# Kernel tuning notes

Hardware: AMD Instinct MI355X
Metric: run time of the kernel (lower is better)

## Reference

```python
import jax, jax.numpy as jnp
import numpy as np

L, H, NH, NKV, HD, FF, V = 2, 2048, 16, 2, 128, 11008, 32000
B, S, R, LORA_SCALE = 32, 64, 16, 2.0  # lora scaling = alpha/r = 32/16
PH, TD = 1024, 512
ROPE_THETA = 1e6

def _rms(x, w, eps=1e-6):
    return x * jax.lax.rsqrt(jnp.mean(x * x, axis=-1, keepdims=True) + eps) * w

def _rot_half(x):
    h = x.shape[-1] // 2
    return jnp.concatenate([-x[..., h:], x[..., :h]], axis=-1)

def _lora_linear(x, W, A, Bm, b=None):
    y = x @ W.T + LORA_SCALE * ((x @ A.T) @ Bm.T)
    return y + b if b is not None else y

def _forward(input_ids, attention_mask, embed, Wq, bq, Aq, Bq, Wk, bk, Ak, Bk,
             Wv, bv, Av, Bv, Wo, Ao, Bo, ln1, ln2, Wg, Wu, Wd, norm_f,
             W1, b1, W2, b2):
    Bsz, Sl = input_ids.shape
    h = embed[input_ids]                                            # [B,S,H]
    inv_freq = 1.0 / (ROPE_THETA ** (jnp.arange(0, HD, 2, dtype=jnp.float32) / HD))
    ang = jnp.arange(Sl, dtype=jnp.float32)[:, None] * inv_freq      # [S,HD/2]
    cos = jnp.concatenate([jnp.cos(ang)] * 2, -1)[None, :, None, :]  # [1,S,1,HD]
    sin = jnp.concatenate([jnp.sin(ang)] * 2, -1)[None, :, None, :]
    causal = jnp.tril(jnp.ones((Sl, Sl), dtype=bool))
    keep = causal[None, None] & (attention_mask[:, None, None, :] > 0)
    bias = jnp.where(keep, 0.0, -1e9).astype(jnp.float32)            # [B,1,S,S]
    for l in range(L):
        x = _rms(h, ln1[l])
        q = _lora_linear(x, Wq[l], Aq[l], Bq[l], bq[l]).reshape(Bsz, Sl, NH, HD)
        k = _lora_linear(x, Wk[l], Ak[l], Bk[l], bk[l]).reshape(Bsz, Sl, NKV, HD)
        v = _lora_linear(x, Wv[l], Av[l], Bv[l], bv[l]).reshape(Bsz, Sl, NKV, HD)
        q = q * cos + _rot_half(q) * sin
        k = k * cos + _rot_half(k) * sin
        k = jnp.repeat(k, NH // NKV, axis=2)                         # GQA expand
        v = jnp.repeat(v, NH // NKV, axis=2)
        scores = jnp.einsum('bqhd,bkhd->bhqk', q, k) / np.sqrt(HD).astype(np.float32) + bias
        p = jax.nn.softmax(scores, axis=-1)
        attn = jnp.einsum('bhqk,bkhd->bqhd', p, v).reshape(Bsz, Sl, H)
        h = h + _lora_linear(attn, Wo[l], Ao[l], Bo[l])
        x = _rms(h, ln2[l])
        h = h + (jax.nn.silu(x @ Wg[l].T) * (x @ Wu[l].T)) @ Wd[l].T  # SwiGLU MLP
    h = _rms(h, norm_f)                       # final norm -> hidden_states[-1]
    seq_len = jnp.sum(attention_mask, axis=1) - 1
    pooled = h[jnp.arange(Bsz), seq_len]      # last valid token  [B,H]
    z = jax.nn.gelu(pooled @ W1.T + b1, approximate=False)
    return (z @ W2.T + b2).astype(jnp.float32)  # [B,512]

def setup_inputs():
    key = jax.random.key(0)
    ks = jax.random.split(key, 32)
    def n(k, shape, s=0.02):
        return (s * jax.random.normal(k, shape)).astype(jnp.float32)
    lens = jax.random.randint(ks[0], (B,), 1, S + 1)
    return {
        'input_ids': jax.random.randint(ks[1], (B, S), 0, V, dtype=jnp.int32),
        'attention_mask': (jnp.arange(S)[None, :] < lens[:, None]).astype(jnp.int32),
        'embed': n(ks[2], (V, H)),
        'Wq': n(ks[3], (L, H, H)), 'bq': n(ks[4], (L, H)),
        'Aq': n(ks[5], (L, R, H)), 'Bq': n(ks[6], (L, H, R)),
        'Wk': n(ks[7], (L, NKV * HD, H)), 'bk': n(ks[8], (L, NKV * HD)),
        'Ak': n(ks[9], (L, R, H)), 'Bk': n(ks[10], (L, NKV * HD, R)),
        'Wv': n(ks[11], (L, NKV * HD, H)), 'bv': n(ks[12], (L, NKV * HD)),
        'Av': n(ks[13], (L, R, H)), 'Bv': n(ks[14], (L, NKV * HD, R)),
        'Wo': n(ks[15], (L, H, H)),
        'Ao': n(ks[16], (L, R, H)), 'Bo': n(ks[17], (L, H, R)),
        'ln1': jnp.ones((L, H), jnp.float32), 'ln2': jnp.ones((L, H), jnp.float32),
        'Wg': n(ks[18], (L, FF, H)), 'Wu': n(ks[19], (L, FF, H)), 'Wd': n(ks[20], (L, H, FF)),
        'norm_f': jnp.ones((H,), jnp.float32),
        'W1': n(ks[21], (PH, H)), 'b1': jnp.zeros((PH,), jnp.float32),
        'W2': n(ks[22], (TD, PH)), 'b2': jnp.zeros((TD,), jnp.float32),
    }

def reference(input_ids, attention_mask, embed, Wq, bq, Aq, Bq, Wk, bk, Ak, Bk,
              Wv, bv, Av, Bv, Wo, Ao, Bo, ln1, ln2, Wg, Wu, Wd, norm_f,
              W1, b1, W2, b2):
    return _forward(input_ids, attention_mask, embed, Wq, bq, Aq, Bq, Wk, bk, Ak, Bk,
                    Wv, bv, Av, Bv, Wo, Ao, Bo, ln1, ln2, Wg, Wu, Wd, norm_f,
                    W1, b1, W2, b2)
```

## Files before the change

kernel.cpp:

```cpp
#include <hip/hip_runtime.h>
#include <hip/hip_bf16.h>
#include <math.h>

namespace {
constexpr int NL  = 2;
constexpr int H   = 2048;
constexpr int NH  = 16;
constexpr int NKV = 2;
constexpr int HD  = 128;
constexpr int FF  = 11008;
constexpr int BB  = 32;
constexpr int SS  = 64;
constexpr int RR  = 16;
constexpr int TT  = BB * SS;
constexpr int KVD = NKV * HD;
constexpr int QKVD = H + 2 * KVD;
constexpr int PH  = 1024, TDm = 512;
constexpr float LSCALE = 2.0f;
}

typedef __bf16 bf16x8 __attribute__((ext_vector_type(8)));
typedef float  f32x4  __attribute__((ext_vector_type(4)));

__device__ __forceinline__ ushort4 f4_to_bf4(float4 r) {
  __hip_bfloat16 a = __float2bfloat16(r.x), b = __float2bfloat16(r.y),
                 c = __float2bfloat16(r.z), d = __float2bfloat16(r.w);
  return make_ushort4(*(unsigned short*)&a, *(unsigned short*)&b,
                      *(unsigned short*)&c, *(unsigned short*)&d);
}

__global__ __launch_bounds__(256) void k_embed(const int* __restrict__ ids,
                                               const float* __restrict__ emb,
                                               float* __restrict__ h) {
  int t = blockIdx.x;
  long id = ids[t];
  const float4* src = reinterpret_cast<const float4*>(emb + id * (long)H);
  float4* dst = reinterpret_cast<float4*>(h + (long)t * H);
  for (int i = threadIdx.x; i < H / 4; i += 256) dst[i] = src[i];
}

__global__ __launch_bounds__(256) void k_cvt(const float* __restrict__ src,
                                             __hip_bfloat16* __restrict__ dst, long n) {
  long i = ((long)blockIdx.x * 256 + threadIdx.x) * 4;
  if (i >= n) return;
  float4 v = *reinterpret_cast<const float4*>(src + i);
  *reinterpret_cast<ushort4*>(dst + i) = f4_to_bf4(v);
}

__global__ __launch_bounds__(256) void k_rmsnorm(const float* __restrict__ in,
                                                 const float* __restrict__ w,
                                                 float* __restrict__ out,
                                                 __hip_bfloat16* __restrict__ outb) {
  int t = blockIdx.x, tid = threadIdx.x;
  const float4* xr = reinterpret_cast<const float4*>(in + (long)t * H);
  float4 v0 = xr[tid], v1 = xr[tid + 256];
  float ss = v0.x*v0.x + v0.y*v0.y + v0.z*v0.z + v0.w*v0.w
           + v1.x*v1.x + v1.y*v1.y + v1.z*v1.z + v1.w*v1.w;
  #pragma unroll
  for (int off = 32; off; off >>= 1) ss += __shfl_xor(ss, off);
  __shared__ float sred[4];
  if ((tid & 63) == 0) sred[tid >> 6] = ss;
  __syncthreads();
  float scale = rsqrtf((sred[0] + sred[1] + sred[2] + sred[3]) * (1.0f / H) + 1e-6f);
  const float4* wr = reinterpret_cast<const float4*>(w);
  float4 w0 = wr[tid], w1 = wr[tid + 256];
  float4 r0 = make_float4(v0.x*scale*w0.x, v0.y*scale*w0.y, v0.z*scale*w0.z, v0.w*scale*w0.w);
  float4 r1 = make_float4(v1.x*scale*w1.x, v1.y*scale*w1.y, v1.z*scale*w1.z, v1.w*scale*w1.w);
  float4* o = reinterpret_cast<float4*>(out + (long)t * H);
  o[tid] = r0; o[tid + 256] = r1;
  ushort4* ob = reinterpret_cast<ushort4*>(outb + (long)t * H);
  ob[tid] = f4_to_bf4(r0); ob[tid + 256] = f4_to_bf4(r1);
}

enum { ME_BIAS_F32 = 0, ME_ACC_F32 = 1, ME_SILU_BF16 = 2, ME_MUL_BF16 = 3 };

__device__ __forceinline__ int raster_sw(int bid, int nwg) {
  int q8 = nwg >> 3, r8 = nwg & 7;
  int xcd = bid & 7, pos = bid >> 3;
  return (xcd < r8 ? xcd * (q8 + 1) : r8 * (q8 + 1) + (xcd - r8) * q8) + pos;
}

template <int EPI>
__global__ __launch_bounds__(512) void k_mgemm(
    const __hip_bfloat16* __restrict__ Abf,
    const __hip_bfloat16* __restrict__ Wbf,
    const float* __restrict__ bias,
    float* __restrict__ Cf,
    __hip_bfloat16* Cb,
    const __hip_bfloat16* gate,
    int M, int N, int K) {
  constexpr int BM = 128, BN = 128, BK = 32;
  constexpr int FM = 4, FN = 2;
  constexpr int ACH = BM * BK / 8, BCH = BN * BK / 8;
  __shared__ __align__(16) __bf16 As[2][BM * BK];
  __shared__ __align__(16) __bf16 Bs[2][BN * BK];
  const int tid = threadIdx.x;
  const int sw = raster_sw(blockIdx.x, gridDim.x);
  const int ntm = M / BM;
  const int bm = (sw % ntm) * BM, bn = (sw / ntm) * BN;
  const int lane = tid & 63, wv = tid >> 6;
  const int wm = (wv >> 2) * 64, wn = (wv & 3) * 32;
  const int lr15 = lane & 15;
  const int lks = (((lane >> 4) << 3)) ^ ((((lr15 >> 1) & 3)) << 3);
  f32x4 acc[FM][FN] = {};
  const __bf16* Ag = reinterpret_cast<const __bf16*>(Abf) + (long)bm * K;
  const __bf16* Bg = reinterpret_cast<const __bf16*>(Wbf) + (long)bn * K;

  auto stage = [&](int buf, int k0) {
    #pragma unroll
    for (int i = tid; i < ACH; i += 512)
      __builtin_amdgcn_global_load_lds(
          (const __attribute__((address_space(1))) void*)
            (Ag + (long)(i >> 2) * K + k0 + (((i & 3) ^ ((i >> 3) & 3)) << 3)),
          (__attribute__((address_space(3))) void*)(&As[buf][i * 8]), 16, 0, 0);
    #pragma unroll
    for (int i = tid; i < BCH; i += 512)
      __builtin_amdgcn_global_load_lds(
          (const __attribute__((address_space(1))) void*)
            (Bg + (long)(i >> 2) * K + k0 + (((i & 3) ^ ((i >> 3) & 3)) << 3)),
          (__attribute__((address_space(3))) void*)(&Bs[buf][i * 8]), 16, 0, 0);
  };
  auto compute = [&](int buf) {
    bf16x8 af[FM], bfr[FN];
    #pragma unroll
    for (int m = 0; m < FM; ++m)
      af[m] = *reinterpret_cast<const bf16x8*>(&As[buf][(wm + m * 16 + lr15) * BK + lks]);
    #pragma unroll
    for (int n = 0; n < FN; ++n)
      bfr[n] = *reinterpret_cast<const bf16x8*>(&Bs[buf][(wn + n * 16 + lr15) * BK + lks]);
    #pragma unroll
    for (int m = 0; m < FM; ++m)
      #pragma unroll
      for (int n = 0; n < FN; ++n)
        acc[m][n] = __builtin_amdgcn_mfma_f32_16x16x32_bf16(af[m], bfr[n], acc[m][n], 0, 0, 0);
  };

  stage(0, 0);
  asm volatile("s_waitcnt vmcnt(0)" ::: "memory");
  __builtin_amdgcn_s_barrier();
  int cur = 0;
  for (int k0 = BK; k0 < K; k0 += BK) {
    stage(cur ^ 1, k0);
    compute(cur);
    asm volatile("s_waitcnt vmcnt(0)" ::: "memory");
    __builtin_amdgcn_s_barrier();
    cur ^= 1;
  }
  compute(cur);

  const int r0 = (lane >> 4) << 2;
  #pragma unroll
  for (int m = 0; m < FM; ++m)
    #pragma unroll
    for (int n = 0; n < FN; ++n) {
      const int col = bn + wn + n * 16 + lr15;
      const long rowb = bm + wm + m * 16 + r0;
      #pragma unroll
      for (int j = 0; j < 4; ++j) {
        const long off = (rowb + j) * N + col;
        float v = acc[m][n][j];
        if constexpr (EPI == ME_BIAS_F32) {
          Cf[off] = v + bias[col];
        } else if constexpr (EPI == ME_ACC_F32) {
          Cf[off] += v;
        } else if constexpr (EPI == ME_SILU_BF16) {
          Cb[off] = __float2bfloat16(v / (1.0f + expf(-v)));
        } else {
          float g = __bfloat162float(gate[off]);
          Cb[off] = __float2bfloat16(v * g);
        }
      }
    }
}

template <int BM, int BN, int WROWS, int WCOLS>
__global__ __launch_bounds__(256, 2) void k_swiglu(
    const __hip_bfloat16* __restrict__ Abf,
    const __hip_bfloat16* __restrict__ Wgb,
    const __hip_bfloat16* __restrict__ Wub,
    __hip_bfloat16* __restrict__ Cb,
    int M, int N, int K) {
  constexpr int BK = 32;
  constexpr int WTM = BM / WROWS, WTN = BN / WCOLS;
  constexpr int FM = WTM / 16, FN = WTN / 16;
  constexpr int ACH = BM * BK / 8, BCH = BN * BK / 8;
  __shared__ __align__(16) __bf16 As[2][BM * BK];
  __shared__ __align__(16) __bf16 Gs[2][BN * BK];
  __shared__ __align__(16) __bf16 Us[2][BN * BK];
  const int tid = threadIdx.x;
  const int sw = raster_sw(blockIdx.x, gridDim.x);
  const int ntm = M / BM;
  const int bm = (sw % ntm) * BM, bn = (sw / ntm) * BN;
  const int lane = tid & 63, wv = tid >> 6;
  const int wm = (wv / WCOLS) * WTM, wn = (wv % WCOLS) * WTN;
  const int lr15 = lane & 15;
  const int lks = (((lane >> 4) << 3)) ^ ((((lr15 >> 1) & 3)) << 3);
  f32x4 accg[FM][FN] = {}, accu[FM][FN] = {};
  const __bf16* Ag = reinterpret_cast<const __bf16*>(Abf) + (long)bm * K;
  const __bf16* Gg = reinterpret_cast<const __bf16*>(Wgb) + (long)bn * K;
  const __bf16* Ug = reinterpret_cast<const __bf16*>(Wub) + (long)bn * K;

  auto stage = [&](int buf, int k0) {
    #pragma unroll
    for (int i = tid; i < ACH; i += 256)
      __builtin_amdgcn_global_load_lds(
          (const __attribute__((address_space(1))) void*)
            (Ag + (long)(i >> 2) * K + k0 + (((i & 3) ^ ((i >> 3) & 3)) << 3)),
          (__attribute__((address_space(3))) void*)(&As[buf][i * 8]), 16, 0, 0);
    #pragma unroll
    for (int i = tid; i < BCH; i += 256)
      __builtin_amdgcn_global_load_lds(
          (const __attribute__((address_space(1))) void*)
            (Gg + (long)(i >> 2) * K + k0 + (((i & 3) ^ ((i >> 3) & 3)) << 3)),
          (__attribute__((address_space(3))) void*)(&Gs[buf][i * 8]), 16, 0, 0);
    #pragma unroll
    for (int i = tid; i < BCH; i += 256)
      __builtin_amdgcn_global_load_lds(
          (const __attribute__((address_space(1))) void*)
            (Ug + (long)(i >> 2) * K + k0 + (((i & 3) ^ ((i >> 3) & 3)) << 3)),
          (__attribute__((address_space(3))) void*)(&Us[buf][i * 8]), 16, 0, 0);
  };
  auto compute = [&](int buf) {
    bf16x8 af[FM], gf[FN], uf[FN];
    #pragma unroll
    for (int m = 0; m < FM; ++m)
      af[m] = *reinterpret_cast<const bf16x8*>(&As[buf][(wm + m * 16 + lr15) * BK + lks]);
    #pragma unroll
    for (int n = 0; n < FN; ++n) {
      gf[n] = *reinterpret_cast<const bf16x8*>(&Gs[buf][(wn + n * 16 + lr15) * BK + lks]);
      uf[n] = *reinterpret_cast<const bf16x8*>(&Us[buf][(wn + n * 16 + lr15) * BK + lks]);
    }
    #pragma unroll
    for (int m = 0; m < FM; ++m)
      #pragma unroll
      for (int n = 0; n < FN; ++n) {
        accg[m][n] = __builtin_amdgcn_mfma_f32_16x16x32_bf16(af[m], gf[n], accg[m][n], 0, 0, 0);
        accu[m][n] = __builtin_amdgcn_mfma_f32_16x16x32_bf16(af[m], uf[n], accu[m][n], 0, 0, 0);
      }
  };

  stage(0, 0);
  asm volatile("s_waitcnt vmcnt(0)" ::: "memory");
  __builtin_amdgcn_s_barrier();
  int cur = 0;
  for (int k0 = BK; k0 < K; k0 += BK) {
    stage(cur ^ 1, k0);
    compute(cur);
    asm volatile("s_waitcnt vmcnt(0)" ::: "memory");
    __builtin_amdgcn_s_barrier();
    cur ^= 1;
  }
  compute(cur);

  const int r0 = (lane >> 4) << 2;
  #pragma unroll
  for (int m = 0; m < FM; ++m)
    #pragma unroll
    for (int n = 0; n < FN; ++n) {
      const int col = bn + wn + n * 16 + lr15;
      const long rowb = bm + wm + m * 16 + r0;
      #pragma unroll
      for (int j = 0; j < 4; ++j) {
        float g = accg[m][n][j], u = accu[m][n][j];
        Cb[(rowb + j) * N + col] = __float2bfloat16((g / (1.0f + expf(-g))) * u);
      }
    }
}

enum { EPI_STORE = 0, EPI_GELU = 3 };

template <int EPI, bool HAS_BIAS>
__global__ __launch_bounds__(256) void k_gemm(const float* __restrict__ A,
                                              const float* __restrict__ W,
                                              const float* __restrict__ bias,
                                              float* __restrict__ C,
                                              int M, int N, int K) {
  constexpr int BM = 64, BN = 64, BK = 16;
  __shared__ float As[BK][BM + 4];
  __shared__ float Ws[BK][BN + 4];
  const int bm = blockIdx.y * BM, bn = blockIdx.x * BN;
  const int tid = threadIdx.x;
  const int lr = tid >> 2;
  const int lc = (tid & 3) << 2;
  const int ty = tid >> 4, tx = tid & 15;
  float acc[4][4] = {};
  const int arow = bm + lr;
  const bool aok = arow < M;
  const float* Ap = A + (long)arow * K + lc;
  const float* Wp = W + (long)(bn + lr) * K + lc;
  for (int k0 = 0; k0 < K; k0 += BK) {
    float4 av = aok ? *reinterpret_cast<const float4*>(Ap + k0) : make_float4(0.f, 0.f, 0.f, 0.f);
    float4 wv = *reinterpret_cast<const float4*>(Wp + k0);
    As[lc + 0][lr] = av.x; As[lc + 1][lr] = av.y; As[lc + 2][lr] = av.z; As[lc + 3][lr] = av.w;
    Ws[lc + 0][lr] = wv.x; Ws[lc + 1][lr] = wv.y; Ws[lc + 2][lr] = wv.z; Ws[lc + 3][lr] = wv.w;
    __syncthreads();
    #pragma unroll
    for (int k = 0; k < BK; ++k) {
      float4 a4 = *reinterpret_cast<const float4*>(&As[k][ty << 2]);
      float4 b4 = *reinterpret_cast<const float4*>(&Ws[k][tx << 2]);
      float a[4] = {a4.x, a4.y, a4.z, a4.w};
      float b[4] = {b4.x, b4.y, b4.z, b4.w};
      #pragma unroll
      for (int i = 0; i < 4; ++i)
        #pragma unroll
        for (int j = 0; j < 4; ++j) acc[i][j] = fmaf(a[i], b[j], acc[i][j]);
    }
    __syncthreads();
  }
  const int col = bn + (tx << 2);
  #pragma unroll
  for (int i = 0; i < 4; ++i) {
    int row = bm + (ty << 2) + i;
    if (row < M) {
      float4 r = make_float4(acc[i][0], acc[i][1], acc[i][2], acc[i][3]);
      if (HAS_BIAS) {
        float4 bv = *reinterpret_cast<const float4*>(bias + col);
        r.x += bv.x; r.y += bv.y; r.z += bv.z; r.w += bv.w;
      }
      if (EPI == EPI_GELU) {
        r.x = 0.5f * r.x * (1.0f + erff(r.x * 0.70710678118654752f));
        r.y = 0.5f * r.y * (1.0f + erff(r.y * 0.70710678118654752f));
        r.z = 0.5f * r.z * (1.0f + erff(r.z * 0.70710678118654752f));
        r.w = 0.5f * r.w * (1.0f + erff(r.w * 0.70710678118654752f));
      }
      *reinterpret_cast<float4*>(C + (long)row * N + col) = r;
    }
  }
}

__global__ __launch_bounds__(256) void k_lora_down(const float* __restrict__ x,
                                                   const float* __restrict__ A,
                                                   float* __restrict__ tmp) {
  int t = blockIdx.x, tid = threadIdx.x;
  int r = tid & 15, sl = tid >> 4;
  const float* xr = x + (long)t * H + sl * 128;
  const float* Ar = A + (long)r * H + sl * 128;
  float p = 0.f;
  #pragma unroll 8
  for (int kk = 0; kk < 128; kk += 4) {
    float4 xv = *reinterpret_cast<const float4*>(xr + kk);
    float4 av = *reinterpret_cast<const float4*>(Ar + kk);
    p = fmaf(xv.x, av.x, p); p = fmaf(xv.y, av.y, p);
    p = fmaf(xv.z, av.z, p); p = fmaf(xv.w, av.w, p);
  }
  __shared__ float red[16][17];
  red[sl][r] = p;
  __syncthreads();
  if (tid < 16) {
    float s = 0.f;
    #pragma unroll
    for (int i = 0; i < 16; ++i) s += red[i][tid];
    tmp[t * RR + tid] = s;
  }
}

__global__ __launch_bounds__(256) void k_lora_add(const float* __restrict__ tmp,
                                                  const float* __restrict__ Bm,
                                                  float* __restrict__ C, int ldC, int N) {
  long idx = (long)blockIdx.x * 256 + threadIdx.x;
  if (idx >= (long)TT * N) return;
  int t = (int)(idx / N), n = (int)(idx % N);
  const float* tr = tmp + (long)t * RR;
  const float* br = Bm + (long)n * RR;
  float s = 0.f;
  #pragma unroll
  for (int r = 0; r < RR; ++r) s = fmaf(tr[r], br[r], s);
  C[(long)t * ldC + n] += LSCALE * s;
}

__global__ __launch_bounds__(256) void k_rope_tab(float2* __restrict__ tab) {
  int idx = blockIdx.x * 256 + threadIdx.x;
  if (idx >= SS * 64) return;
  int pos = idx >> 6, j = idx & 63;
  float inv = 1.0f / powf(1.0e6f, (float)(2 * j) * (1.0f / HD));
  float ang = (float)pos * inv;
  tab[idx] = make_float2(cosf(ang), sinf(ang));
}

__global__ __launch_bounds__(256) void k_rope(float* __restrict__ qkv,
                                              const float2* __restrict__ tab) {
  int t = blockIdx.x;
  const float2* trow = tab + (t & (SS - 1)) * 64;
  float* row = qkv + (long)t * QKVD;
  for (int idx = threadIdx.x; idx < NH * 64 + NKV * 64; idx += 256) {
    float* base;
    int j;
    if (idx < NH * 64) {
      int head = idx >> 6; j = idx & 63;
      base = row + head * HD;
    } else {
      int i2 = idx - NH * 64;
      int head = i2 >> 6; j = i2 & 63;
      base = row + H + head * HD;
    }
    float2 cs2 = trow[j];
    float lo = base[j], hi = base[j + 64];
    base[j]      = lo * cs2.x - hi * cs2.y;
    base[j + 64] = hi * cs2.x + lo * cs2.y;
  }
}

__global__ __launch_bounds__(64) void k_attn(const float* __restrict__ qkv,
                                             const int* __restrict__ mask,
                                             float* __restrict__ o,
                                             __hip_bfloat16* __restrict__ obf) {
  int flat = blockIdx.x;
  int qi = flat & (SS - 1);
  int hh = (flat >> 6) & (NH - 1);
  int b  = flat >> 10;
  int lane = threadIdx.x;
  int kv = hh >> 3;
  long t = (long)b * SS + qi;
  const float* qr = qkv + t * QKVD + hh * HD;
  const float* kr = qkv + ((long)b * SS + lane) * QKVD + H + kv * HD;
  float dot = 0.f;
  #pragma unroll 8
  for (int d = 0; d < HD; d += 4) {
    float4 qv = *reinterpret_cast<const float4*>(qr + d);
    float4 kvv = *reinterpret_cast<const float4*>(kr + d);
    dot = fmaf(qv.x, kvv.x, dot); dot = fmaf(qv.y, kvv.y, dot);
    dot = fmaf(qv.z, kvv.z, dot); dot = fmaf(qv.w, kvv.w, dot);
  }
  bool keep = (lane <= qi) && (mask[b * SS + lane] > 0);
  float sc = dot * 0.08838834764831845f + (keep ? 0.f : -1e9f);
  float m = sc;
  #pragma unroll
  for (int off = 32; off; off >>= 1) m = fmaxf(m, __shfl_xor(m, off));
  float e = expf(sc - m);
  float s = e;
  #pragma unroll
  for (int off = 32; off; off >>= 1) s += __shfl_xor(s, off);
  float p = e / s;
  __shared__ float pl[64];
  pl[lane] = p;
  __syncthreads();
  float o0 = 0.f, o1 = 0.f;
  const float* vb = qkv + (long)b * SS * QKVD + H + KVD + kv * HD;
  for (int ki = 0; ki < SS; ++ki) {
    float pp = pl[ki];
    o0 = fmaf(pp, vb[(long)ki * QKVD + lane], o0);
    o1 = fmaf(pp, vb[(long)ki * QKVD + lane + 64], o1);
  }
  long oidx = t * H + hh * HD + lane;
  o[oidx] = o0;
  o[oidx + 64] = o1;
  __hip_bfloat16 b0 = __float2bfloat16(o0), b1 = __float2bfloat16(o1);
  obf[oidx] = b0;
  obf[oidx + 64] = b1;
}

__global__ __launch_bounds__(256) void k_pool(const float* __restrict__ x,
                                              const int* __restrict__ mask,
                                              float* __restrict__ pooled) {
  int b = blockIdx.x;
  __shared__ int len;
  if (threadIdx.x == 0) {
    int L2 = 0;
    for (int i = 0; i < SS; ++i) L2 += (mask[b * SS + i] > 0);
    len = L2;
  }
  __syncthreads();
  const float4* sp = reinterpret_cast<const float4*>(x + ((long)b * SS + len - 1) * H);
  float4* dp = reinterpret_cast<float4*>(pooled + (long)b * H);
  for (int i = threadIdx.x; i < H / 4; i += 256) dp[i] = sp[i];
}

static inline int cvt_grid(long n) { return (int)((n / 4 + 255) / 256); }

extern "C" void kernel_launch(void* const* d_in, const int* in_sizes, int n_in,
                              void* d_out, int out_size, void* d_ws, size_t ws_size,
                              hipStream_t stream) {
  const int*   ids    = (const int*)d_in[0];
  const int*   mask   = (const int*)d_in[1];
  const float* embed  = (const float*)d_in[2];
  const float* Wq     = (const float*)d_in[3];
  const float* bq     = (const float*)d_in[4];
  const float* Aq     = (const float*)d_in[5];
  const float* Bq     = (const float*)d_in[6];
  const float* Wk     = (const float*)d_in[7];
  const float* bk     = (const float*)d_in[8];
  const float* Ak     = (const float*)d_in[9];
  const float* Bk     = (const float*)d_in[10];
  const float* Wv     = (const float*)d_in[11];
  const float* bv     = (const float*)d_in[12];
  const float* Av     = (const float*)d_in[13];
  const float* Bv     = (const float*)d_in[14];
  const float* Wo     = (const float*)d_in[15];
  const float* Ao     = (const float*)d_in[16];
  const float* Bo     = (const float*)d_in[17];
  const float* ln1    = (const float*)d_in[18];
  const float* ln2    = (const float*)d_in[19];
  const float* Wg     = (const float*)d_in[20];
  const float* Wu     = (const float*)d_in[21];
  const float* Wd     = (const float*)d_in[22];
  const float* norm_f = (const float*)d_in[23];
  const float* W1     = (const float*)d_in[24];
  const float* b1     = (const float*)d_in[25];
  const float* W2     = (const float*)d_in[26];
  const float* b2     = (const float*)d_in[27];

  float* ws = (float*)d_ws;
  float* h       = ws;
  float* x       = h    + (long)TT * H;
  float* qkv     = x    + (long)TT * H;
  float* tmpR    = qkv  + (long)TT * QKVD;
  float* pooled  = tmpR + (long)TT * RR;
  float* zz      = pooled + (long)BB * H;
  float* biascat = zz   + (long)BB * PH;
  float2* ropetab = (float2*)(biascat + QKVD);
  float* endf32  = (float*)(ropetab + SS * 64);
  __hip_bfloat16* x_bf = (__hip_bfloat16*)endf32;
  __hip_bfloat16* ffbf = x_bf + (long)TT * H;
  __hip_bfloat16* wbf  = ffbf + (long)TT * FF;
  __hip_bfloat16* wbf2 = wbf  + (long)FF * H;
  size_t need_fused = (size_t)((char*)(wbf2 + (long)FF * H) - (char*)d_ws);
  bool fused_ok = ws_size >= need_fused;

  k_embed<<<TT, 256, 0, stream>>>(ids, embed, h);
  k_rope_tab<<<(SS * 64 + 255) / 256, 256, 0, stream>>>(ropetab);

  for (int l = 0; l < NL; ++l) {
    const long lHH = (long)l * H * H;
    const long lKH = (long)l * KVD * H;
    const long lRH = (long)l * RR * H;
    k_rmsnorm<<<TT, 256, 0, stream>>>(h, ln1 + l * H, x, x_bf);
    k_cvt<<<cvt_grid((long)H * H), 256, 0, stream>>>(Wq + lHH, wbf, (long)H * H);
    k_cvt<<<cvt_grid((long)KVD * H), 256, 0, stream>>>(Wk + lKH, wbf + (long)H * H, (long)KVD * H);
    k_cvt<<<cvt_grid((long)KVD * H), 256, 0, stream>>>(Wv + lKH, wbf + (long)(H + KVD) * H, (long)KVD * H);
    hipMemcpyAsync(biascat,           bq + (long)l * H,   H * sizeof(float),   hipMemcpyDeviceToDevice, stream);
    hipMemcpyAsync(biascat + H,       bk + (long)l * KVD, KVD * sizeof(float), hipMemcpyDeviceToDevice, stream);
    hipMemcpyAsync(biascat + H + KVD, bv + (long)l * KVD, KVD * sizeof(float), hipMemcpyDeviceToDevice, stream);
    k_mgemm<ME_BIAS_F32><<<(TT / 128) * (QKVD / 128), 512, 0, stream>>>(
        x_bf, wbf, biascat, qkv, nullptr, nullptr, TT, QKVD, H);
    k_lora_down<<<TT, 256, 0, stream>>>(x, Aq + lRH, tmpR);
    k_lora_add<<<((long)TT * H + 255) / 256, 256, 0, stream>>>(tmpR, Bq + (long)l * H * RR, qkv, QKVD, H);
    k_lora_down<<<TT, 256, 0, stream>>>(x, Ak + lRH, tmpR);
    k_lora_add<<<((long)TT * KVD + 255) / 256, 256, 0, stream>>>(tmpR, Bk + (long)l * KVD * RR, qkv + H, QKVD, KVD);
    k_lora_down<<<TT, 256, 0, stream>>>(x, Av + lRH, tmpR);
    k_lora_add<<<((long)TT * KVD + 255) / 256, 256, 0, stream>>>(tmpR, Bv + (long)l * KVD * RR, qkv + H + KVD, QKVD, KVD);
    k_rope<<<TT, 256, 0, stream>>>(qkv, ropetab);
    k_attn<<<BB * NH * SS, 64, 0, stream>>>(qkv, mask, x, x_bf);
    k_lora_down<<<TT, 256, 0, stream>>>(x, Ao + lRH, tmpR);
    k_cvt<<<cvt_grid((long)H * H), 256, 0, stream>>>(Wo + lHH, wbf, (long)H * H);
    k_mgemm<ME_ACC_F32><<<(TT / 128) * (H / 128), 512, 0, stream>>>(
        x_bf, wbf, nullptr, h, nullptr, nullptr, TT, H, H);
    k_lora_add<<<((long)TT * H + 255) / 256, 256, 0, stream>>>(tmpR, Bo + (long)l * H * RR, h, H, H);
    k_rmsnorm<<<TT, 256, 0, stream>>>(h, ln2 + l * H, x, x_bf);
    if (fused_ok) {
      k_cvt<<<cvt_grid((long)FF * H), 256, 0, stream>>>(Wg + (long)l * FF * H, wbf, (long)FF * H);
      k_cvt<<<cvt_grid((long)FF * H), 256, 0, stream>>>(Wu + (long)l * FF * H, wbf2, (long)FF * H);
      k_swiglu<128, 128, 2, 2><<<(TT / 128) * (FF / 128), 256, 0, stream>>>(
          x_bf, wbf, wbf2, ffbf, TT, FF, H);
    } else {
      k_cvt<<<cvt_grid((long)FF * H), 256, 0, stream>>>(Wg + (long)l * FF * H, wbf, (long)FF * H);
      k_mgemm<ME_SILU_BF16><<<(TT / 128) * (FF / 128), 512, 0, stream>>>(
          x_bf, wbf, nullptr, nullptr, ffbf, nullptr, TT, FF, H);
      k_cvt<<<cvt_grid((long)FF * H), 256, 0, stream>>>(Wu + (long)l * FF * H, wbf, (long)FF * H);
      k_mgemm<ME_MUL_BF16><<<(TT / 128) * (FF / 128), 512, 0, stream>>>(
          x_bf, wbf, nullptr, nullptr, ffbf, ffbf, TT, FF, H);
    }
    k_cvt<<<cvt_grid((long)H * FF), 256, 0, stream>>>(Wd + (long)l * H * FF, wbf, (long)H * FF);
    k_mgemm<ME_ACC_F32><<<(TT / 128) * (H / 128), 512, 0, stream>>>(
        ffbf, wbf, nullptr, h, nullptr, nullptr, TT, H, FF);
  }

  k_rmsnorm<<<TT, 256, 0, stream>>>(h, norm_f, x, x_bf);
  k_pool<<<BB, 256, 0, stream>>>(x, mask, pooled);
  k_gemm<EPI_GELU, true><<<dim3(PH / 64, 1), 256, 0, stream>>>(pooled, W1, b1, zz, BB, PH, H);
  k_gemm<EPI_STORE, true><<<dim3(TDm / 64, 1), 256, 0, stream>>>(zz, W2, b2, (float*)d_out, BB, TDm, PH);
}
```

Baseline: 2.117 ms.

## Convert fp32 weights to bf16 inside GEMM staging and fuse LoRA up-projection into epilogue

```diff
diff --git a/kernel.cpp b/kernel.cpp
--- a/kernel.cpp
+++ b/kernel.cpp
@@ -29,6 +29,17 @@
                       *(unsigned short*)&c, *(unsigned short*)&d);
 }
 
+__device__ __forceinline__ bf16x8 f8cvt(float4 a, float4 b) {
+  bf16x8 r;
+  r[0] = (__bf16)a.x; r[1] = (__bf16)a.y; r[2] = (__bf16)a.z; r[3] = (__bf16)a.w;
+  r[4] = (__bf16)b.x; r[5] = (__bf16)b.y; r[6] = (__bf16)b.z; r[7] = (__bf16)b.w;
+  return r;
+}
+
+__device__ __forceinline__ float dot4(float4 a, float4 b) {
+  return a.x * b.x + a.y * b.y + a.z * b.z + a.w * b.w;
+}
+
 __global__ __launch_bounds__(256) void k_embed(const int* __restrict__ ids,
                                                const float* __restrict__ emb,
                                                float* __restrict__ h) {
@@ -39,12 +50,20 @@
   for (int i = threadIdx.x; i < H / 4; i += 256) dst[i] = src[i];
 }
 
-__global__ __launch_bounds__(256) void k_cvt(const float* __restrict__ src,
-                                             __hip_bfloat16* __restrict__ dst, long n) {
-  long i = ((long)blockIdx.x * 256 + threadIdx.x) * 4;
-  if (i >= n) return;
-  float4 v = *reinterpret_cast<const float4*>(src + i);
-  *reinterpret_cast<ushort4*>(dst + i) = f4_to_bf4(v);
+__global__ __launch_bounds__(256) void k_prep(
+    const float* __restrict__ bq, const float* __restrict__ bk, const float* __restrict__ bv,
+    const float* __restrict__ Bq, const float* __restrict__ Bk, const float* __restrict__ Bv,
+    float* __restrict__ biascat, float* __restrict__ bcat) {
+  int idx = blockIdx.x * 256 + threadIdx.x;
+  if (idx >= NL * QKVD) return;
+  int l = idx / QKVD, col = idx % QKVD;
+  const float* bsrc; const float* Bsrc;
+  if (col < H)            { bsrc = bq + (long)l * H + col;            Bsrc = Bq + ((long)l * H + col) * RR; }
+  else if (col < H + KVD) { bsrc = bk + (long)l * KVD + (col - H);    Bsrc = Bk + ((long)l * KVD + col - H) * RR; }
+  else                    { bsrc = bv + (long)l * KVD + (col - H - KVD); Bsrc = Bv + ((long)l * KVD + col - H - KVD) * RR; }
+  biascat[idx] = *bsrc;
+  #pragma unroll
+  for (int r = 0; r < RR; ++r) bcat[(long)idx * RR + r] = Bsrc[r];
 }
 
 __global__ __launch_bounds__(256) void k_rmsnorm(const float* __restrict__ in,
@@ -72,7 +91,7 @@
   ob[tid] = f4_to_bf4(r0); ob[tid + 256] = f4_to_bf4(r1);
 }
 
-enum { ME_BIAS_F32 = 0, ME_ACC_F32 = 1, ME_SILU_BF16 = 2, ME_MUL_BF16 = 3 };
+enum { ME_BIAS_F32 = 0, ME_ACC_F32 = 1 };
 
 __device__ __forceinline__ int raster_sw(int bid, int nwg) {
   int q8 = nwg >> 3, r8 = nwg & 7;
@@ -80,18 +99,16 @@
   return (xcd < r8 ? xcd * (q8 + 1) : r8 * (q8 + 1) + (xcd - r8) * q8) + pos;
 }
 
-template <int EPI>
+template <int EPI, bool LORA>
 __global__ __launch_bounds__(512) void k_mgemm(
     const __hip_bfloat16* __restrict__ Abf,
-    const __hip_bfloat16* __restrict__ Wbf,
+    const float* __restrict__ W0, const float* __restrict__ W1, const float* __restrict__ W2,
     const float* __restrict__ bias,
     float* __restrict__ Cf,
-    __hip_bfloat16* Cb,
-    const __hip_bfloat16* gate,
-    int M, int N, int K) {
+    const float* __restrict__ lt, const float* __restrict__ lB, int ltStride,
+    int qkvMode, int M, int N, int K) {
   constexpr int BM = 128, BN = 128, BK = 32;
   constexpr int FM = 4, FN = 2;
-  constexpr int ACH = BM * BK / 8, BCH = BN * BK / 8;
   __shared__ __align__(16) __bf16 As[2][BM * BK];
   __shared__ __align__(16) __bf16 Bs[2][BN * BK];
   const int tid = threadIdx.x;
@@ -104,21 +121,29 @@
   const int lks = (((lane >> 4) << 3)) ^ ((((lr15 >> 1) & 3)) << 3);
   f32x4 acc[FM][FN] = {};
   const __bf16* Ag = reinterpret_cast<const __bf16*>(Abf) + (long)bm * K;
-  const __bf16* Bg = reinterpret_cast<const __bf16*>(Wbf) + (long)bn * K;
-
-  auto stage = [&](int buf, int k0) {
-    #pragma unroll
-    for (int i = tid; i < ACH; i += 512)
-      __builtin_amdgcn_global_load_lds(
-          (const __attribute__((address_space(1))) void*)
-            (Ag + (long)(i >> 2) * K + k0 + (((i & 3) ^ ((i >> 3) & 3)) << 3)),
-          (__attribute__((address_space(3))) void*)(&As[buf][i * 8]), 16, 0, 0);
-    #pragma unroll
-    for (int i = tid; i < BCH; i += 512)
-      __builtin_amdgcn_global_load_lds(
-          (const __attribute__((address_space(1))) void*)
-            (Bg + (long)(i >> 2) * K + k0 + (((i & 3) ^ ((i >> 3) & 3)) << 3)),
-          (__attribute__((address_space(3))) void*)(&Bs[buf][i * 8]), 16, 0, 0);
+
+  const float* Wsrc = W0; int wrow0 = bn;
+  if (qkvMode) {
+    if (bn >= H + KVD)      { Wsrc = W2; wrow0 = bn - (H + KVD); }
+    else if (bn >= H)       { Wsrc = W1; wrow0 = bn - H; }
+  }
+  const int brow = tid >> 2, bc = tid & 3;
+  const float* wp = Wsrc + (long)(wrow0 + brow) * K + bc * 8;
+  const int bdst = brow * BK + ((bc ^ ((brow >> 1) & 3)) << 3);
+
+  float4 b0, b1;
+  auto loadB = [&](int k0) {
+    b0 = *reinterpret_cast<const float4*>(wp + k0);
+    b1 = *reinterpret_cast<const float4*>(wp + k0 + 4);
+  };
+  auto writeB = [&](int buf) {
+    *reinterpret_cast<bf16x8*>(&Bs[buf][bdst]) = f8cvt(b0, b1);
+  };
+  auto stageA = [&](int buf, int k0) {
+    __builtin_amdgcn_global_load_lds(
+        (const __attribute__((address_space(1))) void*)
+          (Ag + (long)(tid >> 2) * K + k0 + (((tid & 3) ^ ((tid >> 3) & 3)) << 3)),
+        (__attribute__((address_space(3))) void*)(&As[buf][tid * 8]), 16, 0, 0);
   };
   auto compute = [&](int buf) {
     bf16x8 af[FM], bfr[FN];
@@ -135,55 +160,71 @@
         acc[m][n] = __builtin_amdgcn_mfma_f32_16x16x32_bf16(af[m], bfr[n], acc[m][n], 0, 0, 0);
   };
 
-  stage(0, 0);
-  asm volatile("s_waitcnt vmcnt(0)" ::: "memory");
-  __builtin_amdgcn_s_barrier();
+  const int NS = K / BK;
+  loadB(0);
+  stageA(0, 0);
+  writeB(0);
+  __syncthreads();
   int cur = 0;
-  for (int k0 = BK; k0 < K; k0 += BK) {
-    stage(cur ^ 1, k0);
+  for (int t = 0; t < NS; ++t) {
+    if (t + 1 < NS) { loadB((t + 1) * BK); stageA(cur ^ 1, (t + 1) * BK); }
     compute(cur);
-    asm volatile("s_waitcnt vmcnt(0)" ::: "memory");
-    __builtin_amdgcn_s_barrier();
-    cur ^= 1;
-  }
-  compute(cur);
+    if (t + 1 < NS) {
+      writeB(cur ^ 1);
+      __syncthreads();
+      cur ^= 1;
+    }
+  }
 
   const int r0 = (lane >> 4) << 2;
+  float4 lb[FN][4];
+  int goff = 0;
+  if constexpr (LORA) {
+    if (qkvMode) goff = (bn >= H + KVD) ? 32 : (bn >= H ? 16 : 0);
+    #pragma unroll
+    for (int n = 0; n < FN; ++n) {
+      const float4* p = reinterpret_cast<const float4*>(lB + (long)(bn + wn + n * 16 + lr15) * RR);
+      lb[n][0] = p[0]; lb[n][1] = p[1]; lb[n][2] = p[2]; lb[n][3] = p[3];
+    }
+  }
+  float bcol[FN];
+  if constexpr (EPI == ME_BIAS_F32) {
+    #pragma unroll
+    for (int n = 0; n < FN; ++n) bcol[n] = bias[bn + wn + n * 16 + lr15];
+  }
   #pragma unroll
   for (int m = 0; m < FM; ++m)
     #pragma unroll
-    for (int n = 0; n < FN; ++n) {
-      const int col = bn + wn + n * 16 + lr15;
-      const long rowb = bm + wm + m * 16 + r0;
+    for (int j = 0; j < 4; ++j) {
+      const long row = bm + wm + m * 16 + r0 + j;
+      float lv[FN];
+      if constexpr (LORA) {
+        const float4* tp = reinterpret_cast<const float4*>(lt + row * ltStride + goff);
+        float4 t0 = tp[0], t1 = tp[1], t2 = tp[2], t3 = tp[3];
+        #pragma unroll
+        for (int n = 0; n < FN; ++n)
+          lv[n] = LSCALE * (dot4(t0, lb[n][0]) + dot4(t1, lb[n][1]) +
+                            dot4(t2, lb[n][2]) + dot4(t3, lb[n][3]));
+      }
       #pragma unroll
-      for (int j = 0; j < 4; ++j) {
-        const long off = (rowb + j) * N + col;
+      for (int n = 0; n < FN; ++n) {
+        const int col = bn + wn + n * 16 + lr15;
         float v = acc[m][n][j];
-        if constexpr (EPI == ME_BIAS_F32) {
-          Cf[off] = v + bias[col];
-        } else if constexpr (EPI == ME_ACC_F32) {
-          Cf[off] += v;
-        } else if constexpr (EPI == ME_SILU_BF16) {
-          Cb[off] = __float2bfloat16(v / (1.0f + expf(-v)));
-        } else {
-          float g = __bfloat162float(gate[off]);
-          Cb[off] = __float2bfloat16(v * g);
-        }
+        if constexpr (LORA) v += lv[n];
+        if constexpr (EPI == ME_BIAS_F32) Cf[row * N + col] = v + bcol[n];
+        else                              Cf[row * N + col] += v;
       }
     }
 }
 
-template <int BM, int BN, int WROWS, int WCOLS>
 __global__ __launch_bounds__(256, 2) void k_swiglu(
     const __hip_bfloat16* __restrict__ Abf,
-    const __hip_bfloat16* __restrict__ Wgb,
-    const __hip_bfloat16* __restrict__ Wub,
+    const float* __restrict__ Wg,
+    const float* __restrict__ Wu,
     __hip_bfloat16* __restrict__ Cb,
     int M, int N, int K) {
-  constexpr int BK = 32;
-  constexpr int WTM = BM / WROWS, WTN = BN / WCOLS;
-  constexpr int FM = WTM / 16, FN = WTN / 16;
-  constexpr int ACH = BM * BK / 8, BCH = BN * BK / 8;
+  constexpr int BM = 128, BN = 128, BK = 32;
+  constexpr int FM = 4, FN = 4;
   __shared__ __align__(16) __bf16 As[2][BM * BK];
   __shared__ __align__(16) __bf16 Gs[2][BN * BK];
   __shared__ __align__(16) __bf16 Us[2][BN * BK];
@@ -192,33 +233,45 @@
   const int ntm = M / BM;
   const int bm = (sw % ntm) * BM, bn = (sw / ntm) * BN;
   const int lane = tid & 63, wv = tid >> 6;
-  const int wm = (wv / WCOLS) * WTM, wn = (wv % WCOLS) * WTN;
+  const int wm = (wv >> 1) * 64, wn = (wv & 1) * 64;
   const int lr15 = lane & 15;
   const int lks = (((lane >> 4) << 3)) ^ ((((lr15 >> 1) & 3)) << 3);
   f32x4 accg[FM][FN] = {}, accu[FM][FN] = {};
   const __bf16* Ag = reinterpret_cast<const __bf16*>(Abf) + (long)bm * K;
-  const __bf16* Gg = reinterpret_cast<const __bf16*>(Wgb) + (long)bn * K;
-  const __bf16* Ug = reinterpret_cast<const __bf16*>(Wub) + (long)bn * K;
-
-  auto stage = [&](int buf, int k0) {
-    #pragma unroll
-    for (int i = tid; i < ACH; i += 256)
+
+  const int br0 = tid >> 2, bc = tid & 3;
+  const int br1 = br0 + 64;
+  const float* gp0 = Wg + (long)(bn + br0) * K + bc * 8;
+  const float* gp1 = Wg + (long)(bn + br1) * K + bc * 8;
+  const float* up0 = Wu + (long)(bn + br0) * K + bc * 8;
+  const float* up1 = Wu + (long)(bn + br1) * K + bc * 8;
+  const int d0 = br0 * BK + ((bc ^ ((br0 >> 1) & 3)) << 3);
+  const int d1 = br1 * BK + ((bc ^ ((br1 >> 1) & 3)) << 3);
+
+  float4 g00, g01, g10, g11, u00, u01, u10, u11;
+  auto loadB = [&](int k0) {
+    g00 = *reinterpret_cast<const float4*>(gp0 + k0);
+    g01 = *reinterpret_cast<const float4*>(gp0 + k0 + 4);
+    g10 = *reinterpret_cast<const float4*>(gp1 + k0);
+    g11 = *reinterpret_cast<const float4*>(gp1 + k0 + 4);
+    u00 = *reinterpret_cast<const float4*>(up0 + k0);
+    u01 = *reinterpret_cast<const float4*>(up0 + k0 + 4);
+    u10 = *reinterpret_cast<const float4*>(up1 + k0);
+    u11 = *reinterpret_cast<const float4*>(up1 + k0 + 4);
+  };
+  auto writeB = [&](int buf) {
+    *reinterpret_cast<bf16x8*>(&Gs[buf][d0]) = f8cvt(g00, g01);
+    *reinterpret_cast<bf16x8*>(&Gs[buf][d1]) = f8cvt(g10, g11);
+    *reinterpret_cast<bf16x8*>(&Us[buf][d0]) = f8cvt(u00, u01);
+    *reinterpret_cast<bf16x8*>(&Us[buf][d1]) = f8cvt(u10, u11);
+  };
+  auto stageA = [&](int buf, int k0) {
+    #pragma unroll
+    for (int i = tid; i < BM * BK / 8; i += 256)
       __builtin_amdgcn_global_load_lds(
           (const __attribute__((address_space(1))) void*)
             (Ag + (long)(i >> 2) * K + k0 + (((i & 3) ^ ((i >> 3) & 3)) << 3)),
           (__attribute__((address_space(3))) void*)(&As[buf][i * 8]), 16, 0, 0);
-    #pragma unroll
-    for (int i = tid; i < BCH; i += 256)
-      __builtin_amdgcn_global_load_lds(
-          (const __attribute__((address_space(1))) void*)
-            (Gg + (long)(i >> 2) * K + k0 + (((i & 3) ^ ((i >> 3) & 3)) << 3)),
-          (__attribute__((address_space(3))) void*)(&Gs[buf][i * 8]), 16, 0, 0);
-    #pragma unroll
-    for (int i = tid; i < BCH; i += 256)
-      __builtin_amdgcn_global_load_lds(
-          (const __attribute__((address_space(1))) void*)
-            (Ug + (long)(i >> 2) * K + k0 + (((i & 3) ^ ((i >> 3) & 3)) << 3)),
-          (__attribute__((address_space(3))) void*)(&Us[buf][i * 8]), 16, 0, 0);
   };
   auto compute = [&](int buf) {
     bf16x8 af[FM], gf[FN], uf[FN];
@@ -239,18 +292,21 @@
       }
   };
 
-  stage(0, 0);
-  asm volatile("s_waitcnt vmcnt(0)" ::: "memory");
-  __builtin_amdgcn_s_barrier();
+  const int NS = K / BK;
+  loadB(0);
+  stageA(0, 0);
+  writeB(0);
+  __syncthreads();
   int cur = 0;
-  for (int k0 = BK; k0 < K; k0 += BK) {
-    stage(cur ^ 1, k0);
+  for (int t = 0; t < NS; ++t) {
+    if (t + 1 < NS) { loadB((t + 1) * BK); stageA(cur ^ 1, (t + 1) * BK); }
     compute(cur);
-    asm volatile("s_waitcnt vmcnt(0)" ::: "memory");
-    __builtin_amdgcn_s_barrier();
-    cur ^= 1;
-  }
-  compute(cur);
+    if (t + 1 < NS) {
+      writeB(cur ^ 1);
+      __syncthreads();
+      cur ^= 1;
+    }
+  }
 
   const int r0 = (lane >> 4) << 2;
   #pragma unroll
@@ -328,10 +384,12 @@
   }
 }
 
-__global__ __launch_bounds__(256) void k_lora_down(const float* __restrict__ x,
-                                                   const float* __restrict__ A,
-                                                   float* __restrict__ tmp) {
-  int t = blockIdx.x, tid = threadIdx.x;
+__global__ __launch_bounds__(256) void k_lora_down3(
+    const float* __restrict__ x,
+    const float* __restrict__ A0, const float* __restrict__ A1, const float* __restrict__ A2,
+    float* __restrict__ out, int outStride) {
+  int t = blockIdx.x, g = blockIdx.y, tid = threadIdx.x;
+  const float* A = (g == 0) ? A0 : (g == 1) ? A1 : A2;
   int r = tid & 15, sl = tid >> 4;
   const float* xr = x + (long)t * H + sl * 128;
   const float* Ar = A + (long)r * H + sl * 128;
@@ -350,22 +408,8 @@
     float s = 0.f;
     #pragma unroll
     for (int i = 0; i < 16; ++i) s += red[i][tid];
-    tmp[t * RR + tid] = s;
-  }
-}
-
-__global__ __launch_bounds__(256) void k_lora_add(const float* __restrict__ tmp,
-                                                  const float* __restrict__ Bm,
-                                                  float* __restrict__ C, int ldC, int N) {
-  long idx = (long)blockIdx.x * 256 + threadIdx.x;
-  if (idx >= (long)TT * N) return;
-  int t = (int)(idx / N), n = (int)(idx % N);
-  const float* tr = tmp + (long)t * RR;
-  const float* br = Bm + (long)n * RR;
-  float s = 0.f;
-  #pragma unroll
-  for (int r = 0; r < RR; ++r) s = fmaf(tr[r], br[r], s);
-  C[(long)t * ldC + n] += LSCALE * s;
+    out[(long)t * outStride + g * 16 + tid] = s;
+  }
 }
 
 __global__ __launch_bounds__(256) void k_rope_tab(float2* __restrict__ tab) {
@@ -464,8 +508,6 @@
   float4* dp = reinterpret_cast<float4*>(pooled + (long)b * H);
   for (int i = threadIdx.x; i < H / 4; i += 256) dp[i] = sp[i];
 }
-
-static inline int cvt_grid(long n) { return (int)((n / 4 + 255) / 256); }
 
 extern "C" void kernel_launch(void* const* d_in, const int* in_sizes, int n_in,
                               void* d_out, int out_size, void* d_ws, size_t ws_size,
@@ -500,68 +542,48 @@
   const float* b2     = (const float*)d_in[27];
 
   float* ws = (float*)d_ws;
-  float* h       = ws;
-  float* x       = h    + (long)TT * H;
-  float* qkv     = x    + (long)TT * H;
-  float* tmpR    = qkv  + (long)TT * QKVD;
-  float* pooled  = tmpR + (long)TT * RR;
-  float* zz      = pooled + (long)BB * H;
-  float* biascat = zz   + (long)BB * PH;
-  float2* ropetab = (float2*)(biascat + QKVD);
-  float* endf32  = (float*)(ropetab + SS * 64);
+  float* h        = ws;
+  float* x        = h    + (long)TT * H;
+  float* qkv      = x    + (long)TT * H;
+  float* tmpR     = qkv  + (long)TT * QKVD;
+  float* tmpO     = tmpR + (long)TT * 48;
+  float* pooled   = tmpO + (long)TT * 16;
+  float* zz       = pooled + (long)BB * H;
+  float* biascat  = zz   + (long)BB * PH;
+  float* bcat     = biascat + (long)NL * QKVD;
+  float2* ropetab = (float2*)(bcat + (long)NL * QKVD * RR);
+  float* endf32   = (float*)(ropetab + SS * 64);
   __hip_bfloat16* x_bf = (__hip_bfloat16*)endf32;
   __hip_bfloat16* ffbf = x_bf + (long)TT * H;
-  __hip_bfloat16* wbf  = ffbf + (long)TT * FF;
-  __hip_bfloat16* wbf2 = wbf  + (long)FF * H;
-  size_t need_fused = (size_t)((char*)(wbf2 + (long)FF * H) - (char*)d_ws);
-  bool fused_ok = ws_size >= need_fused;
 
   k_embed<<<TT, 256, 0, stream>>>(ids, embed, h);
   k_rope_tab<<<(SS * 64 + 255) / 256, 256, 0, stream>>>(ropetab);
+  k_prep<<<(NL * QKVD + 255) / 256, 256, 0, stream>>>(bq, bk, bv, Bq, Bk, Bv, biascat, bcat);
 
   for (int l = 0; l < NL; ++l) {
     const long lHH = (long)l * H * H;
     const long lKH = (long)l * KVD * H;
     const long lRH = (long)l * RR * H;
+    const long lFH = (long)l * FF * H;
     k_rmsnorm<<<TT, 256, 0, stream>>>(h, ln1 + l * H, x, x_bf);
-    k_cvt<<<cvt_grid((long)H * H), 256, 0, stream>>>(Wq + lHH, wbf, (long)H * H);
-    k_cvt<<<cvt_grid((long)KVD * H), 256, 0, stream>>>(Wk + lKH, wbf + (long)H * H, (long)KVD * H);
-    k_cvt<<<cvt_grid((long)KVD * H), 256, 0, stream>>>(Wv + lKH, wbf + (long)(H + KVD) * H, (long)KVD * H);
-    hipMemcpyAsync(biascat,           bq + (long)l * H,   H * sizeof(float),   hipMemcpyDeviceToDevice, stream);
-    hipMemcpyAsync(biascat + H,       bk + (long)l * KVD, KVD * sizeof(float), hipMemcpyDeviceToDevice, stream);
-    hipMemcpyAsync(biascat + H + KVD, bv + (long)l * KVD, KVD * sizeof(float), hipMemcpyDeviceToDevice, stream);
-    k_mgemm<ME_BIAS_F32><<<(TT / 128) * (QKVD / 128), 512, 0, stream>>>(
-        x_bf, wbf, biascat, qkv, nullptr, nullptr, TT, QKVD, H);
-    k_lora_down<<<TT, 256, 0, stream>>>(x, Aq + lRH, tmpR);
-    k_lora_add<<<((long)TT * H + 255) / 256, 256, 0, stream>>>(tmpR, Bq + (long)l * H * RR, qkv, QKVD, H);
-    k_lora_down<<<TT, 256, 0, stream>>>(x, Ak + lRH, tmpR);
-    k_lora_add<<<((long)TT * KVD + 255) / 256, 256, 0, stream>>>(tmpR, Bk + (long)l * KVD * RR, qkv + H, QKVD, KVD);
-    k_lora_down<<<TT, 256, 0, stream>>>(x, Av + lRH, tmpR);
-    k_lora_add<<<((long)TT * KVD + 255) / 256, 256, 0, stream>>>(tmpR, Bv + (long)l * KVD * RR, qkv + H + KVD, QKVD, KVD);
+    k_lora_down3<<<dim3(TT, 3), 256, 0, stream>>>(
+        x, Aq + lRH, Ak + lRH, Av + lRH, tmpR, 48);
+    k_mgemm<ME_BIAS_F32, true><<<(TT / 128) * (QKVD / 128), 512, 0, stream>>>(
+        x_bf, Wq + lHH, Wk + lKH, Wv + lKH, biascat + (long)l * QKVD, qkv,
+        tmpR, bcat + (long)l * QKVD * RR, 48, 1, TT, QKVD, H);
     k_rope<<<TT, 256, 0, stream>>>(qkv, ropetab);
     k_attn<<<BB * NH * SS, 64, 0, stream>>>(qkv, mask, x, x_bf);
-    k_lora_down<<<TT, 256, 0, stream>>>(x, Ao + lRH, tmpR);
-    k_cvt<<<cvt_grid((long)H * H), 256, 0, stream>>>(Wo + lHH, wbf, (long)H * H);
-    k_mgemm<ME_ACC_F32><<<(TT / 128) * (H / 128), 512, 0, stream>>>(
-        x_bf, wbf, nullptr, h, nullptr, nullptr, TT, H, H);
-    k_lora_add<<<((long)TT * H + 255) / 256, 256, 0, stream>>>(tmpR, Bo + (long)l * H * RR, h, H, H);
+    k_lora_down3<<<dim3(TT, 1), 256, 0, stream>>>(
+        x, Ao + lRH, Ao + lRH, Ao + lRH, tmpO, 16);
+    k_mgemm<ME_ACC_F32, true><<<(TT / 128) * (H / 128), 512, 0, stream>>>(
+        x_bf, Wo + lHH, Wo + lHH, Wo + lHH, nullptr, h,
+        tmpO, Bo + (long)l * H * RR, 16, 0, TT, H, H);
     k_rmsnorm<<<TT, 256, 0, stream>>>(h, ln2 + l * H, x, x_bf);
-    if (fused_ok) {
-      k_cvt<<<cvt_grid((long)FF * H), 256, 0, stream>>>(Wg + (long)l * FF * H, wbf, (long)FF * H);
-      k_cvt<<<cvt_grid((long)FF * H), 256, 0, stream>>>(Wu + (long)l * FF * H, wbf2, (long)FF * H);
-      k_swiglu<128, 128, 2, 2><<<(TT / 128) * (FF / 128), 256, 0, stream>>>(
-          x_bf, wbf, wbf2, ffbf, TT, FF, H);
-    } else {
-      k_cvt<<<cvt_grid((long)FF * H), 256, 0, stream>>>(Wg + (long)l * FF * H, wbf, (long)FF * H);
-      k_mgemm<ME_SILU_BF16><<<(TT / 128) * (FF / 128), 512, 0, stream>>>(
-          x_bf, wbf, nullptr, nullptr, ffbf, nullptr, TT, FF, H);
-      k_cvt<<<cvt_grid((long)FF * H), 256, 0, stream>>>(Wu + (long)l * FF * H, wbf, (long)FF * H);
-      k_mgemm<ME_MUL_BF16><<<(TT / 128) * (FF / 128), 512, 0, stream>>>(
-          x_bf, wbf, nullptr, nullptr, ffbf, ffbf, TT, FF, H);
-    }
-    k_cvt<<<cvt_grid((long)H * FF), 256, 0, stream>>>(Wd + (long)l * H * FF, wbf, (long)H * FF);
-    k_mgemm<ME_ACC_F32><<<(TT / 128) * (H / 128), 512, 0, stream>>>(
-        ffbf, wbf, nullptr, h, nullptr, nullptr, TT, H, FF);
+    k_swiglu<<<(TT / 128) * (FF / 128), 256, 0, stream>>>(
+        x_bf, Wg + lFH, Wu + lFH, ffbf, TT, FF, H);
+    k_mgemm<ME_ACC_F32, false><<<(TT / 128) * (H / 128), 512, 0, stream>>>(
+        ffbf, Wd + lFH, Wd + lFH, Wd + lFH, nullptr, h,
+        nullptr, nullptr, 0, 0, TT, H, FF);
   }
 
   k_rmsnorm<<<TT, 256, 0, stream>>>(h, norm_f, x, x_bf);
```

New measurement: 2.401 ms. 1.13x slower.
